# Optimization experiments

Measured on AMD Instinct MI355X. Metric: run time of the kernel, lower is better.

The kernel has to match this reference:

```python
import jax, jax.numpy as jnp
import numpy as np

NODE_DIM = 128
CTX_DIM = 256
OUT_DIM = 256
GRID_SIZE = 4
SPLINE_ORDER = 3
IN_DIM = 3 * NODE_DIM  # subj + obj + transformed context
N_NODES = 100000
N_EDGES = 100000


def make_grid(in_dim, grid_size, spline_order, grid_range=(-1.0, 1.0)):
    h = (grid_range[1] - grid_range[0]) / grid_size
    g = (np.arange(-spline_order, grid_size + spline_order + 1, dtype=np.float32) * h
         + grid_range[0])  # [grid_size + 2*spline_order + 1]
    return jnp.asarray(np.tile(g[None, :], (in_dim, 1)))  # [in, G]


def b_splines(x, grid, spline_order):
    # x: [N, in], grid: [in, G] -> bases: [N, in, grid_size + spline_order]
    xg = x[:, :, None]
    bases = ((xg >= grid[:, :-1]) & (xg < grid[:, 1:])).astype(x.dtype)
    for k in range(1, spline_order + 1):
        left = (xg - grid[:, : -(k + 1)]) / (grid[:, k:-1] - grid[:, : -(k + 1)]) * bases[..., :-1]
        right = (grid[:, k + 1:] - xg) / (grid[:, k + 1:] - grid[:, 1:-k]) * bases[..., 1:]
        bases = left + right
    return bases


def setup_inputs() -> dict:
    key = jax.random.key(0)
    ks = jax.random.split(key, 8)
    n_coef = GRID_SIZE + SPLINE_ORDER
    return {
        "node_embeddings": jax.random.normal(ks[0], (N_NODES, NODE_DIM), jnp.float32),
        "context_embeddings": jax.random.normal(ks[1], (N_EDGES, CTX_DIM), jnp.float32),
        "pair_indices": jax.random.randint(ks[2], (N_EDGES, 2), 0, N_NODES, jnp.int64 if jax.config.jax_enable_x64 else jnp.int32),
        "ctx_w": jax.random.normal(ks[3], (NODE_DIM, CTX_DIM), jnp.float32) * (1.0 / np.sqrt(CTX_DIM)),
        "ctx_b": jnp.zeros((NODE_DIM,), jnp.float32),
        "base_weight": jax.random.normal(ks[4], (OUT_DIM, IN_DIM), jnp.float32) * (1.0 / np.sqrt(IN_DIM)),
        "spline_weight": jax.random.normal(ks[5], (OUT_DIM, IN_DIM, n_coef), jnp.float32) * 0.1,
        "spline_scaler": jax.random.normal(ks[6], (OUT_DIM, IN_DIM), jnp.float32) * (1.0 / np.sqrt(IN_DIM)),
        "grid": make_grid(IN_DIM, GRID_SIZE, SPLINE_ORDER),
    }


def reference(node_embeddings, context_embeddings, pair_indices, ctx_w, ctx_b,
              base_weight, spline_weight, spline_scaler, grid):
    # gather subject/object node embeddings (irregular access)
    subj = node_embeddings[pair_indices[:, 0]]          # [E, node_dim]
    obj = node_embeddings[pair_indices[:, 1]]           # [E, node_dim]
    ctx = context_embeddings @ ctx_w.T + ctx_b          # [E, node_dim]
    x = jnp.concatenate([subj, obj, ctx], axis=1)       # [E, 3*node_dim]

    # efficient-KAN linear layer: base (SiLU) branch + B-spline branch
    base_out = jax.nn.silu(x) @ base_weight.T           # [E, out]
    bsp = b_splines(x, grid, SPLINE_ORDER)              # [E, in, n_coef]
    scaled_w = spline_weight * spline_scaler[:, :, None]  # [out, in, n_coef]
    spline_out = jnp.einsum('nic,oic->no', bsp, scaled_w)
    return base_out + spline_out
```

## Files before the change

### kernel.cpp

```cpp
#include <hip/hip_runtime.h>

#define NEDGES   100000
#define NODE_DIM 128
#define CTX_DIM  256
#define OUT_DIM  256
#define IN_DIM   384
#define NCOEF    7

#define BM2      128
#define BK2      32
#define NCH2     96
#define THR2     512

typedef __bf16 bf16x8 __attribute__((ext_vector_type(8)));
typedef float  f32x4  __attribute__((ext_vector_type(4)));

static __device__ __forceinline__ unsigned short f2bf(float f) {
    unsigned int u = __float_as_uint(f);
    u += 0x7FFFu + ((u >> 16) & 1u);
    return (unsigned short)(u >> 16);
}
static __device__ __forceinline__ float bf2f(unsigned short h) {
    return __uint_as_float(((unsigned int)h) << 16);
}
static __device__ __forceinline__ unsigned int pkbf(float a, float b) {
    unsigned int ua = __float_as_uint(a), ub = __float_as_uint(b);
    ua += 0x7FFFu + ((ua >> 16) & 1u);
    ub += 0x7FFFu + ((ub >> 16) & 1u);
    return (ua >> 16) | (ub & 0xFFFF0000u);
}
static __device__ __forceinline__ float silu(float x) {
    return x / (1.0f + __expf(-x));
}
static __device__ __forceinline__ float n3(float t) {
    float d2 = t - 2.0f;
    float a  = fabsf(d2);
    float p1 = fmaf(fmaf(0.5f, a, -1.0f), d2 * d2, 0.66666667f);
    float dd = fmaxf(2.0f - a, 0.0f);
    float p2 = dd * dd * (dd * (1.0f / 6.0f));
    return a < 1.0f ? p1 : p2;
}

static __device__ __forceinline__ void glds16(const unsigned short* g, unsigned short* l) {
    __builtin_amdgcn_global_load_lds(
        (const __attribute__((address_space(1))) void*)g,
        (__attribute__((address_space(3))) void*)l, 16, 0, 0);
}

__global__ void prep_w2(const float* __restrict__ base_w,
                        const float* __restrict__ spline_w,
                        const float* __restrict__ spline_s,
                        unsigned short* __restrict__ Wsw)
{
    int o = blockIdx.x;
    int i = threadIdx.x;
    int bi = o * IN_DIM + i;
    float sc = spline_s[bi];
    const float* sw = spline_w + (size_t)bi * NCOEF;
    uint4 v;
    v.x = pkbf(base_w[bi], sw[0] * sc);
    v.y = pkbf(sw[1] * sc, sw[2] * sc);
    v.z = pkbf(sw[3] * sc, sw[4] * sc);
    v.w = pkbf(sw[5] * sc, sw[6] * sc);
    int ch = i >> 2, g8 = i & 3;
    int p  = o * 4 + (((o >> 1) + g8) & 3);
    *(uint4*)(Wsw + (size_t)ch * (OUT_DIM * BK2) + p * 8) = v;
}

#define K1STR 72
#define BM   128
__global__ __launch_bounds__(512, 2)
void build_x(const float* __restrict__ node_emb,
             const float* __restrict__ ctx_emb,
             const int*   __restrict__ pair,
             const float* __restrict__ ctx_w,
             const float* __restrict__ ctx_b,
             unsigned short* __restrict__ Xbf)
{
    __shared__ unsigned short sm[2 * 128 * K1STR];
    const int tid    = threadIdx.x;
    const int e_base = blockIdx.x * BM;
    const int wid    = tid >> 6;
    const int lan    = tid & 63;
    const int lrow   = lan & 15;
    const int lquad  = lan >> 4;

    #pragma unroll
    for (int it = 0; it < 16; ++it) {
        int id    = it * 512 + tid;
        int f4    = id & 31;
        int which = (id >> 5) & 1;
        int e     = id >> 6;
        int eg = e_base + e; if (eg >= NEDGES) eg = NEDGES - 1;
        int node = pair[eg * 2 + which];
        float4 v = *(const float4*)(node_emb + (size_t)node * NODE_DIM + f4 * 4);
        *(uint2*)&Xbf[(size_t)eg * IN_DIM + which * NODE_DIM + f4 * 4] =
            make_uint2(pkbf(v.x, v.y), pkbf(v.z, v.w));
    }

    f32x4 acc[4][2];
    #pragma unroll
    for (int a = 0; a < 4; ++a)
        #pragma unroll
        for (int b = 0; b < 2; ++b) { f32x4 z = {0.f,0.f,0.f,0.f}; acc[a][b] = z; }

    const int m0 = (wid & 1) * 64;
    const int n0 = (wid >> 1) * 32;

    for (int kc = 0; kc < 4; ++kc) {
        #pragma unroll
        for (int it = 0; it < 4; ++it) {
            int id = it * 512 + tid;
            int r  = id >> 4;
            int c4 = id & 15;
            int eg = e_base + r; if (eg >= NEDGES) eg = NEDGES - 1;
            float4 v = *(const float4*)(ctx_emb + (size_t)eg * CTX_DIM + kc * 64 + c4 * 4);
            *(uint2*)&sm[r * K1STR + c4 * 4] = make_uint2(pkbf(v.x, v.y), pkbf(v.z, v.w));
            float4 w = *(const float4*)(ctx_w + (size_t)r * CTX_DIM + kc * 64 + c4 * 4);
            *(uint2*)&sm[128 * K1STR + r * K1STR + c4 * 4] = make_uint2(pkbf(w.x, w.y), pkbf(w.z, w.w));
        }
        __syncthreads();
        #pragma unroll
        for (int ks = 0; ks < 2; ++ks) {
            int koff = ks * 32 + lquad * 8;
            bf16x8 af[4], bfr[2];
            #pragma unroll
            for (int mt = 0; mt < 4; ++mt)
                af[mt] = *(const bf16x8*)&sm[(m0 + mt*16 + lrow) * K1STR + koff];
            #pragma unroll
            for (int nt = 0; nt < 2; ++nt)
                bfr[nt] = *(const bf16x8*)&sm[128 * K1STR + (n0 + nt*16 + lrow) * K1STR + koff];
            #pragma unroll
            for (int mt = 0; mt < 4; ++mt)
                #pragma unroll
                for (int nt = 0; nt < 2; ++nt)
                    acc[mt][nt] = __builtin_amdgcn_mfma_f32_16x16x32_bf16(
                        af[mt], bfr[nt], acc[mt][nt], 0, 0, 0);
        }
        __syncthreads();
    }

    #define ESTR 136
    #pragma unroll
    for (int nt = 0; nt < 2; ++nt) {
        int col = n0 + nt * 16 + lrow;
        float cb = ctx_b[col];
        #pragma unroll
        for (int mt = 0; mt < 4; ++mt)
            #pragma unroll
            for (int r = 0; r < 4; ++r) {
                int row = m0 + mt * 16 + lquad * 4 + r;
                sm[row * ESTR + col] = f2bf(acc[mt][nt][r] + cb);
            }
    }
    __syncthreads();
    #pragma unroll
    for (int it = 0; it < 8; ++it) {
        int id = it * 512 + tid;
        int row = id >> 5;
        int g   = id & 31;
        int eg = e_base + row; if (eg >= NEDGES) eg = NEDGES - 1;
        *(uint2*)&Xbf[(size_t)eg * IN_DIM + 256 + g * 4] = *(uint2*)&sm[row * ESTR + g * 4];
    }
}

#define A2STR  40
#define A2SZ   (BM2 * A2STR)
#define B2SZ   (OUT_DIM * BK2)
#define OFF_A0 0
#define OFF_A1 A2SZ
#define OFF_B0 (2 * A2SZ)
#define OFF_B1 (2 * A2SZ + B2SZ)
#define LDS2   (2 * A2SZ + 2 * B2SZ)

static __device__ __forceinline__ void gen_elem(
    unsigned short xh, float hinv, float b0, unsigned short* dst)
{
    float x  = bf2f(xh);
    float sl = silu(x);
    unsigned short slh = f2bf(sl);
    float t  = fmaf(x, hinv, b0);
    float jf = floorf(t);
    int   j0 = (int)jf;
    float u  = t - jf;
    float u2 = u * u, u3 = u2 * u;
    float Q0 = u3 * 0.16666667f;
    float d  = 1.0f - u;
    float Q3 = d * d * d * 0.16666667f;
    float Q1 = fmaf(0.5f, u + u2 - u3, 0.16666667f);
    float Q2 = fmaf(0.5f, u3, 0.66666667f - u2);
    unsigned plo = pkbf(Q3, Q2);
    unsigned phi = pkbf(Q1, Q0);
    unsigned long long P = ((unsigned long long)phi << 32) | plo;
    int sh = (j0 << 4) - 32;
    unsigned a  = (unsigned)sh;
    unsigned na = 0u - a;
    unsigned long long lo =
        (a  < 64u) ? (P << (a  & 63u)) : ((na < 64u) ? (P >> (na & 63u)) : 0ull);
    unsigned b2 = a - 64u;
    unsigned nb = 0u - b2;
    unsigned long long hi =
        (b2 < 64u) ? (P << (b2 & 63u)) : ((nb < 64u) ? (P >> (nb & 63u)) : 0ull);
    lo = (lo & ~0xFFFFull) | (unsigned long long)slh;
    uint4 w;
    w.x = (unsigned)lo; w.y = (unsigned)(lo >> 32);
    w.z = (unsigned)hi; w.w = (unsigned)(hi >> 32);
    *(uint4*)dst = w;
}

__global__ __launch_bounds__(THR2, 4)
void kan_gemm2(const unsigned short* __restrict__ Wsw,
               const unsigned short* __restrict__ Xbf,
               const float* __restrict__ grid,
               float* __restrict__ out)
{
    __shared__ unsigned short smem[LDS2];
    const int tid    = threadIdx.x;
    const int e_base = blockIdx.x * BM2;
    const int wid    = tid >> 6;
    const int lan    = tid & 63;
    const int lrow   = lan & 15;
    const int lquad  = lan >> 4;
    const int m0     = (wid & 1) * 64;
    const int n0     = (wid >> 1) * 64;

    const float g0   = grid[0];
    const float hinv = 1.0f / (grid[1] - grid[0]);
    const float b0   = -g0 * hinv;

    const int grow = tid >> 2;
    const int gcol = tid & 3;
    int geg = e_base + grow; if (geg >= NEDGES) geg = NEDGES - 1;
    const unsigned short* xp = Xbf + (size_t)geg * IN_DIM + gcol;
    const unsigned awr = grow * A2STR + gcol * 8;

    f32x4 acc[4][4];
    #pragma unroll
    for (int a = 0; a < 4; ++a)
        #pragma unroll
        for (int b = 0; b < 4; ++b) { f32x4 z = {0.f,0.f,0.f,0.f}; acc[a][b] = z; }

    unsigned short xc = xp[0];
    unsigned short xn = xp[4];

    #pragma unroll
    for (int it = 0; it < 2; ++it) {
        int id = it * THR2 + tid;
        glds16(Wsw + id * 8, &smem[OFF_B0 + id * 8]);
    }
    gen_elem(xc, hinv, b0, &smem[OFF_A0 + awr]);
    __syncthreads();

    for (int kb = 0; kb < NCH2; ++kb) {
        const int cur = kb & 1;
        if (kb + 1 < NCH2) {
            const unsigned short* wc = Wsw + (size_t)(kb + 1) * B2SZ;
            unsigned boff = cur ? OFF_B0 : OFF_B1;
            #pragma unroll
            for (int it = 0; it < 2; ++it) {
                int id = it * THR2 + tid;
                glds16(wc + id * 8, &smem[boff + id * 8]);
            }
            unsigned short xh = xn;
            if (kb + 2 < NCH2) xn = xp[(kb + 2) * 4];
            gen_elem(xh, hinv, b0, &smem[(cur ? OFF_A0 : OFF_A1) + awr]);
        }
        const unsigned ab = cur ? OFF_A1 : OFF_A0;
        const unsigned bb = cur ? OFF_B1 : OFF_B0;
        bf16x8 af[4], bfr[4];
        #pragma unroll
        for (int mt = 0; mt < 4; ++mt)
            af[mt] = *(const bf16x8*)&smem[ab + (m0 + mt*16 + lrow) * A2STR + lquad * 8];
        #pragma unroll
        for (int nt = 0; nt < 4; ++nt) {
            int n = n0 + nt * 16 + lrow;
            bfr[nt] = *(const bf16x8*)&smem[bb + n * 32 + ((((n >> 1) + lquad) & 3) << 3)];
        }
        #pragma unroll
        for (int mt = 0; mt < 4; ++mt)
            #pragma unroll
            for (int nt = 0; nt < 4; ++nt)
                acc[mt][nt] = __builtin_amdgcn_mfma_f32_16x16x32_bf16(
                    af[mt], bfr[nt], acc[mt][nt], 0, 0, 0);
        __syncthreads();
    }

    #pragma unroll
    for (int mt = 0; mt < 4; ++mt) {
        #pragma unroll
        for (int r = 0; r < 4; ++r) {
            int row = m0 + mt * 16 + lquad * 4 + r;
            int eg  = e_base + row;
            if (eg < NEDGES) {
                float* op = out + (size_t)eg * OUT_DIM + n0 + lrow;
                #pragma unroll
                for (int nt = 0; nt < 4; ++nt)
                    op[nt * 16] = acc[mt][nt][r];
            }
        }
    }
}

#define XSTR 392
#define FSTR 72
#define FOFF_X 0
#define FOFF_A (128 * XSTR)
#define FOFF_B (FOFF_A + 128 * FSTR)
#define FLDS (FOFF_B + OUT_DIM * FSTR)

__global__ __launch_bounds__(512, 2)
void fused_fallback(const float* __restrict__ node_emb,
                    const float* __restrict__ ctx_emb,
                    const int*   __restrict__ pair,
                    const float* __restrict__ ctx_w,
                    const float* __restrict__ ctx_b,
                    const float* __restrict__ base_w,
                    const float* __restrict__ spline_w,
                    const float* __restrict__ spline_s,
                    const float* __restrict__ grid,
                    float* __restrict__ out)
{
    __shared__ unsigned short smem[FLDS];
    const int tid    = threadIdx.x;
    const int e_base = blockIdx.x * 128;
    const int wid    = tid >> 6;
    const int lan    = tid & 63;
    const int lrow   = lan & 15;
    const int lquad  = lan >> 4;

    #pragma unroll
    for (int it = 0; it < 16; ++it) {
        int id    = it * 512 + tid;
        int lane4 = id & 31;
        int e     = (id >> 5) & 127;
        int which = id >> 12;
        int eg = e_base + e; if (eg >= NEDGES) eg = NEDGES - 1;
        int node = pair[eg * 2 + which];
        const float4 v = *(const float4*)(node_emb + (size_t)node * NODE_DIM + lane4 * 4);
        *(ushort4*)&smem[FOFF_X + e * XSTR + which * NODE_DIM + lane4 * 4] =
            make_ushort4(f2bf(v.x), f2bf(v.y), f2bf(v.z), f2bf(v.w));
    }
    {
        f32x4 cacc[4][2];
        #pragma unroll
        for (int a = 0; a < 4; ++a)
            #pragma unroll
            for (int b = 0; b < 2; ++b) { f32x4 z = {0.f,0.f,0.f,0.f}; cacc[a][b] = z; }
        const int m0 = (wid & 1) * 64;
        const int n0 = (wid >> 1) * 32;
        for (int kc = 0; kc < 4; ++kc) {
            #pragma unroll
            for (int it = 0; it < 4; ++it) {
                int id = it * 512 + tid;
                int r  = id >> 4;
                int c4 = id & 15;
                int eg = e_base + r; if (eg >= NEDGES) eg = NEDGES - 1;
                float4 v = *(const float4*)(ctx_emb + (size_t)eg * CTX_DIM + kc * 64 + c4 * 4);
                *(ushort4*)&smem[FOFF_A + r * FSTR + c4 * 4] =
                    make_ushort4(f2bf(v.x), f2bf(v.y), f2bf(v.z), f2bf(v.w));
                float4 w = *(const float4*)(ctx_w + (size_t)r * CTX_DIM + kc * 64 + c4 * 4);
                *(ushort4*)&smem[FOFF_B + r * FSTR + c4 * 4] =
                    make_ushort4(f2bf(w.x), f2bf(w.y), f2bf(w.z), f2bf(w.w));
            }
            __syncthreads();
            #pragma unroll
            for (int ks = 0; ks < 2; ++ks) {
                int koff = ks * 32 + lquad * 8;
                bf16x8 af[4], bfr[2];
                #pragma unroll
                for (int mt = 0; mt < 4; ++mt)
                    af[mt] = *(const bf16x8*)&smem[FOFF_A + (m0 + mt*16 + lrow) * FSTR + koff];
                #pragma unroll
                for (int nt = 0; nt < 2; ++nt)
                    bfr[nt] = *(const bf16x8*)&smem[FOFF_B + (n0 + nt*16 + lrow) * FSTR + koff];
                #pragma unroll
                for (int mt = 0; mt < 4; ++mt)
                    #pragma unroll
                    for (int nt = 0; nt < 2; ++nt)
                        cacc[mt][nt] = __builtin_amdgcn_mfma_f32_16x16x32_bf16(
                            af[mt], bfr[nt], cacc[mt][nt], 0, 0, 0);
            }
            __syncthreads();
        }
        #pragma unroll
        for (int mt = 0; mt < 4; ++mt)
            #pragma unroll
            for (int nt = 0; nt < 2; ++nt)
                #pragma unroll
                for (int r = 0; r < 4; ++r) {
                    int row = m0 + mt*16 + lquad*4 + r;
                    int col = n0 + nt*16 + lrow;
                    smem[FOFF_X + row * XSTR + 256 + col] = f2bf(cacc[mt][nt][r] + ctx_b[col]);
                }
    }
    __syncthreads();

    const float g0   = grid[0];
    const float hinv = 1.0f / (grid[1] - grid[0]);

    f32x4 acc[4][4];
    #pragma unroll
    for (int a = 0; a < 4; ++a)
        #pragma unroll
        for (int b = 0; b < 4; ++b) { f32x4 z = {0.f,0.f,0.f,0.f}; acc[a][b] = z; }

    const int m0 = (wid & 1) * 64;
    const int n0 = (wid >> 1) * 64;

    for (int kb = 0; kb < 48; ++kb) {
        const int seg = kb / 6;
        const int i0  = (kb - seg * 6) * 64;
        #pragma unroll
        for (int it = 0; it < 4; ++it) {
            int id = it * 512 + tid;
            int e  = id >> 4;
            int qq = id & 15;
            ushort4 xv = *(const ushort4*)&smem[FOFF_X + e * XSTR + i0 + qq * 4];
            float x0 = bf2f(xv.x), x1 = bf2f(xv.y), x2 = bf2f(xv.z), x3 = bf2f(xv.w);
            unsigned short r0, r1, r2, r3;
            if (seg == 0) {
                r0 = f2bf(silu(x0)); r1 = f2bf(silu(x1));
                r2 = f2bf(silu(x2)); r3 = f2bf(silu(x3));
            } else {
                const float cf = (float)(seg - 1);
                r0 = f2bf(n3((x0 - g0) * hinv - cf));
                r1 = f2bf(n3((x1 - g0) * hinv - cf));
                r2 = f2bf(n3((x2 - g0) * hinv - cf));
                r3 = f2bf(n3((x3 - g0) * hinv - cf));
            }
            *(ushort4*)&smem[FOFF_A + e * FSTR + qq * 4] = make_ushort4(r0, r1, r2, r3);
        }
        #pragma unroll
        for (int it = 0; it < 4; ++it) {
            int id = it * 512 + tid;
            int o  = id >> 4;
            int qq = id & 15;
            unsigned short r0, r1, r2, r3;
            if (seg == 0) {
                const float4 w = *(const float4*)(base_w + (size_t)o * IN_DIM + i0 + qq * 4);
                r0 = f2bf(w.x); r1 = f2bf(w.y); r2 = f2bf(w.z); r3 = f2bf(w.w);
            } else {
                int c  = seg - 1;
                int bi = o * IN_DIM + i0 + qq * 4;
                r0 = f2bf(spline_w[(size_t)(bi    ) * NCOEF + c] * spline_s[bi    ]);
                r1 = f2bf(spline_w[(size_t)(bi + 1) * NCOEF + c] * spline_s[bi + 1]);
                r2 = f2bf(spline_w[(size_t)(bi + 2) * NCOEF + c] * spline_s[bi + 2]);
                r3 = f2bf(spline_w[(size_t)(bi + 3) * NCOEF + c] * spline_s[bi + 3]);
            }
            *(ushort4*)&smem[FOFF_B + o * FSTR + qq * 4] = make_ushort4(r0, r1, r2, r3);
        }
        __syncthreads();
        #pragma unroll
        for (int ks = 0; ks < 2; ++ks) {
            int koff = ks * 32 + lquad * 8;
            bf16x8 af[4], bfr[4];
            #pragma unroll
            for (int mt = 0; mt < 4; ++mt)
                af[mt] = *(const bf16x8*)&smem[FOFF_A + (m0 + mt*16 + lrow) * FSTR + koff];
            #pragma unroll
            for (int nt = 0; nt < 4; ++nt)
                bfr[nt] = *(const bf16x8*)&smem[FOFF_B + (n0 + nt*16 + lrow) * FSTR + koff];
            #pragma unroll
            for (int mt = 0; mt < 4; ++mt)
                #pragma unroll
                for (int nt = 0; nt < 4; ++nt)
                    acc[mt][nt] = __builtin_amdgcn_mfma_f32_16x16x32_bf16(
                        af[mt], bfr[nt], acc[mt][nt], 0, 0, 0);
        }
        __syncthreads();
    }

    #pragma unroll
    for (int mt = 0; mt < 4; ++mt) {
        #pragma unroll
        for (int r = 0; r < 4; ++r) {
            int row = m0 + mt*16 + lquad*4 + r;
            int eg  = e_base + row;
            if (eg < NEDGES) {
                float* op = out + (size_t)eg * OUT_DIM + n0 + lrow;
                #pragma unroll
                for (int nt = 0; nt < 4; ++nt)
                    op[nt * 16] = acc[mt][nt][r];
            }
        }
    }
}

extern "C" void kernel_launch(void* const* d_in, const int* in_sizes, int n_in,
                              void* d_out, int out_size, void* d_ws, size_t ws_size,
                              hipStream_t stream)
{
    const float* node_emb = (const float*)d_in[0];
    const float* ctx_emb  = (const float*)d_in[1];
    const int*   pair     = (const int*)d_in[2];
    const float* ctx_w    = (const float*)d_in[3];
    const float* ctx_b    = (const float*)d_in[4];
    const float* base_w   = (const float*)d_in[5];
    const float* spline_w = (const float*)d_in[6];
    const float* spline_s = (const float*)d_in[7];
    const float* grid     = (const float*)d_in[8];
    float* out = (float*)d_out;

    const int nblk = (NEDGES + BM2 - 1) / BM2;
    const size_t xoff = 2u * 1024u * 1024u;
    const size_t need = xoff + (size_t)NEDGES * IN_DIM * sizeof(unsigned short);

    if (ws_size >= need) {
        unsigned short* Wsw = (unsigned short*)d_ws;
        unsigned short* Xbf = (unsigned short*)((char*)d_ws + xoff);
        prep_w2<<<OUT_DIM, IN_DIM, 0, stream>>>(base_w, spline_w, spline_s, Wsw);
        build_x<<<nblk, 512, 0, stream>>>(node_emb, ctx_emb, pair, ctx_w, ctx_b, Xbf);
        kan_gemm2<<<nblk, THR2, 0, stream>>>(Wsw, Xbf, grid, out);
    } else {
        fused_fallback<<<nblk, 512, 0, stream>>>(
            node_emb, ctx_emb, pair, ctx_w, ctx_b, base_w, spline_w, spline_s, grid, out);
    }
}
```

Measured before the change: 440.3 us.

## Split build_x into gather and ctx GEMM kernels with bf16 ctx_w preconversion

```diff
diff --git a/kernel.cpp b/kernel.cpp
--- a/kernel.cpp
+++ b/kernel.cpp
@@ -67,36 +67,51 @@
     *(uint4*)(Wsw + (size_t)ch * (OUT_DIM * BK2) + p * 8) = v;
 }
 
-#define K1STR 72
-#define BM   128
-__global__ __launch_bounds__(512, 2)
-void build_x(const float* __restrict__ node_emb,
-             const float* __restrict__ ctx_emb,
-             const int*   __restrict__ pair,
-             const float* __restrict__ ctx_w,
-             const float* __restrict__ ctx_b,
-             unsigned short* __restrict__ Xbf)
-{
-    __shared__ unsigned short sm[2 * 128 * K1STR];
+__global__ void prep_ctxw(const float* __restrict__ ctx_w,
+                          unsigned short* __restrict__ B)
+{
+    int n  = blockIdx.x;
+    int k4 = threadIdx.x;
+    float4 v = *(const float4*)(ctx_w + (size_t)n * CTX_DIM + k4 * 4);
+    *(uint2*)&B[(size_t)n * CTX_DIM + k4 * 4] =
+        make_uint2(pkbf(v.x, v.y), pkbf(v.z, v.w));
+}
+
+__global__ __launch_bounds__(256)
+void gather_x(const float* __restrict__ node_emb,
+              const int*   __restrict__ pair,
+              unsigned short* __restrict__ Xbf)
+{
+    const int stride = gridDim.x * blockDim.x;
+    const int total  = NEDGES * 64;
+    for (int id = blockIdx.x * blockDim.x + threadIdx.x; id < total; id += stride) {
+        int f4    = id & 31;
+        int which = (id >> 5) & 1;
+        int e     = id >> 6;
+        int node  = pair[e * 2 + which];
+        float4 v = *(const float4*)(node_emb + (size_t)node * NODE_DIM + f4 * 4);
+        *(uint2*)&Xbf[(size_t)e * IN_DIM + which * NODE_DIM + f4 * 4] =
+            make_uint2(pkbf(v.x, v.y), pkbf(v.z, v.w));
+    }
+}
+
+#define CG_STR 72
+#define CG_ESTR 136
+__global__ __launch_bounds__(512, 4)
+void ctx_gemm(const float* __restrict__ ctx_emb,
+              const unsigned short* __restrict__ ctxwB,
+              const float* __restrict__ ctx_b,
+              unsigned short* __restrict__ Xbf)
+{
+    __shared__ unsigned short sm[2 * 128 * CG_STR];
     const int tid    = threadIdx.x;
-    const int e_base = blockIdx.x * BM;
+    const int e_base = blockIdx.x * 128;
     const int wid    = tid >> 6;
     const int lan    = tid & 63;
     const int lrow   = lan & 15;
     const int lquad  = lan >> 4;
-
-    #pragma unroll
-    for (int it = 0; it < 16; ++it) {
-        int id    = it * 512 + tid;
-        int f4    = id & 31;
-        int which = (id >> 5) & 1;
-        int e     = id >> 6;
-        int eg = e_base + e; if (eg >= NEDGES) eg = NEDGES - 1;
-        int node = pair[eg * 2 + which];
-        float4 v = *(const float4*)(node_emb + (size_t)node * NODE_DIM + f4 * 4);
-        *(uint2*)&Xbf[(size_t)eg * IN_DIM + which * NODE_DIM + f4 * 4] =
-            make_uint2(pkbf(v.x, v.y), pkbf(v.z, v.w));
-    }
+    const int m0     = (wid & 1) * 64;
+    const int n0     = (wid >> 1) * 32;
 
     f32x4 acc[4][2];
     #pragma unroll
@@ -104,32 +119,41 @@
         #pragma unroll
         for (int b = 0; b < 2; ++b) { f32x4 z = {0.f,0.f,0.f,0.f}; acc[a][b] = z; }
 
-    const int m0 = (wid & 1) * 64;
-    const int n0 = (wid >> 1) * 32;
+    #pragma unroll
+    for (int it = 0; it < 4; ++it) {
+        int id = it * 512 + tid;
+        int r  = id >> 4;
+        int c4 = id & 15;
+        int eg = e_base + r; if (eg >= NEDGES) eg = NEDGES - 1;
+        float4 v = *(const float4*)(ctx_emb + (size_t)eg * CTX_DIM + c4 * 4);
+        *(uint2*)&sm[r * CG_STR + c4 * 4] = make_uint2(pkbf(v.x, v.y), pkbf(v.z, v.w));
+    }
+    __syncthreads();
 
     for (int kc = 0; kc < 4; ++kc) {
-        #pragma unroll
-        for (int it = 0; it < 4; ++it) {
-            int id = it * 512 + tid;
-            int r  = id >> 4;
-            int c4 = id & 15;
-            int eg = e_base + r; if (eg >= NEDGES) eg = NEDGES - 1;
-            float4 v = *(const float4*)(ctx_emb + (size_t)eg * CTX_DIM + kc * 64 + c4 * 4);
-            *(uint2*)&sm[r * K1STR + c4 * 4] = make_uint2(pkbf(v.x, v.y), pkbf(v.z, v.w));
-            float4 w = *(const float4*)(ctx_w + (size_t)r * CTX_DIM + kc * 64 + c4 * 4);
-            *(uint2*)&sm[128 * K1STR + r * K1STR + c4 * 4] = make_uint2(pkbf(w.x, w.y), pkbf(w.z, w.w));
-        }
-        __syncthreads();
+        if (kc + 1 < 4) {
+            unsigned short* nb = sm + ((kc + 1) & 1) * 128 * CG_STR;
+            #pragma unroll
+            for (int it = 0; it < 4; ++it) {
+                int id = it * 512 + tid;
+                int r  = id >> 4;
+                int c4 = id & 15;
+                int eg = e_base + r; if (eg >= NEDGES) eg = NEDGES - 1;
+                float4 v = *(const float4*)(ctx_emb + (size_t)eg * CTX_DIM + (kc + 1) * 64 + c4 * 4);
+                *(uint2*)&nb[r * CG_STR + c4 * 4] = make_uint2(pkbf(v.x, v.y), pkbf(v.z, v.w));
+            }
+        }
+        const unsigned short* sa = sm + (kc & 1) * 128 * CG_STR;
         #pragma unroll
         for (int ks = 0; ks < 2; ++ks) {
             int koff = ks * 32 + lquad * 8;
             bf16x8 af[4], bfr[2];
             #pragma unroll
             for (int mt = 0; mt < 4; ++mt)
-                af[mt] = *(const bf16x8*)&sm[(m0 + mt*16 + lrow) * K1STR + koff];
+                af[mt] = *(const bf16x8*)&sa[(m0 + mt*16 + lrow) * CG_STR + koff];
             #pragma unroll
             for (int nt = 0; nt < 2; ++nt)
-                bfr[nt] = *(const bf16x8*)&sm[128 * K1STR + (n0 + nt*16 + lrow) * K1STR + koff];
+                bfr[nt] = *(const bf16x8*)&ctxwB[(size_t)(n0 + nt*16 + lrow) * CTX_DIM + kc * 64 + koff];
             #pragma unroll
             for (int mt = 0; mt < 4; ++mt)
                 #pragma unroll
@@ -140,7 +164,6 @@
         __syncthreads();
     }
 
-    #define ESTR 136
     #pragma unroll
     for (int nt = 0; nt < 2; ++nt) {
         int col = n0 + nt * 16 + lrow;
@@ -150,17 +173,17 @@
             #pragma unroll
             for (int r = 0; r < 4; ++r) {
                 int row = m0 + mt * 16 + lquad * 4 + r;
-                sm[row * ESTR + col] = f2bf(acc[mt][nt][r] + cb);
+                sm[row * CG_ESTR + col] = f2bf(acc[mt][nt][r] + cb);
             }
     }
     __syncthreads();
     #pragma unroll
     for (int it = 0; it < 8; ++it) {
-        int id = it * 512 + tid;
+        int id  = it * 512 + tid;
         int row = id >> 5;
         int g   = id & 31;
-        int eg = e_base + row; if (eg >= NEDGES) eg = NEDGES - 1;
-        *(uint2*)&Xbf[(size_t)eg * IN_DIM + 256 + g * 4] = *(uint2*)&sm[row * ESTR + g * 4];
+        int eg  = e_base + row; if (eg >= NEDGES) eg = NEDGES - 1;
+        *(uint2*)&Xbf[(size_t)eg * IN_DIM + 256 + g * 4] = *(uint2*)&sm[row * CG_ESTR + g * 4];
     }
 }
 
@@ -502,14 +525,18 @@
     float* out = (float*)d_out;
 
     const int nblk = (NEDGES + BM2 - 1) / BM2;
-    const size_t xoff = 2u * 1024u * 1024u;
+    const size_t xoff    = 2u * 1024u * 1024u;
+    const size_t ctxwoff = 1572864u;
     const size_t need = xoff + (size_t)NEDGES * IN_DIM * sizeof(unsigned short);
 
     if (ws_size >= need) {
-        unsigned short* Wsw = (unsigned short*)d_ws;
-        unsigned short* Xbf = (unsigned short*)((char*)d_ws + xoff);
+        unsigned short* Wsw   = (unsigned short*)d_ws;
+        unsigned short* CtxwB = (unsigned short*)((char*)d_ws + ctxwoff);
+        unsigned short* Xbf   = (unsigned short*)((char*)d_ws + xoff);
         prep_w2<<<OUT_DIM, IN_DIM, 0, stream>>>(base_w, spline_w, spline_s, Wsw);
-        build_x<<<nblk, 512, 0, stream>>>(node_emb, ctx_emb, pair, ctx_w, ctx_b, Xbf);
+        prep_ctxw<<<128, 64, 0, stream>>>(ctx_w, CtxwB);
+        gather_x<<<2048, 256, 0, stream>>>(node_emb, pair, Xbf);
+        ctx_gemm<<<nblk, 512, 0, stream>>>(ctx_emb, CtxwB, ctx_b, Xbf);
         kan_gemm2<<<nblk, THR2, 0, stream>>>(Wsw, Xbf, grid, out);
     } else {
         fused_fallback<<<nblk, 512, 0, stream>>>(
```

Measured after the change: 453.1 us. 1.03x slower.
